# Kernel tuning notes

Hardware: AMD Instinct MI355X
Metric: run time of the kernel (lower is better)

## Reference

```python
import jax, jax.numpy as jnp
import numpy as np

EPS = 1e-6
D = 100   # embed_dim
P = 10    # perspective


def _cos(v1, v2):
    # cosine over last dim with broadcasting; clamp sum-of-squares at EPS (as torch)
    num = (v1 * v2).sum(-1)
    n1 = jnp.sqrt(jnp.clip((v1 * v1).sum(-1), EPS, None))
    n2 = jnp.sqrt(jnp.clip((v2 * v2).sum(-1), EPS, None))
    return num / (n1 * n2)


def _cosine_matrix(s1, s2):
    # [n1,B,D] x [n2,B,D] -> [n1,n2,B]; einsum avoids the [n1,n2,B,D] intermediate
    num = jnp.einsum('ibd,jbd->ijb', s1, s2)
    n1 = jnp.sqrt(jnp.clip((s1 * s1).sum(-1), EPS, None))  # [n1,B]
    n2 = jnp.sqrt(jnp.clip((s2 * s2).sum(-1), EPS, None))  # [n2,B]
    return num / (n1[:, None] * n2[None])


def _full(s1, s2, w):
    ws1 = s1[:, :, None, :] * w            # [n1,B,P,D]
    ws2 = s2[-1][:, None, :] * w           # [B,P,D]
    return _cos(ws1, ws2[None])            # [n1,B,P]


def _maxpool(s1, s2, w):
    # cos[i,j,b,p] between s1[i,b]*w[p] and s2[j,b]*w[p], without the 5-D intermediate
    w2 = w * w
    num = jnp.einsum('ibd,jbd,pd->ijbp', s1, s2, w2)
    n1 = jnp.sqrt(jnp.clip(jnp.einsum('ibd,pd->ibp', s1 * s1, w2), EPS, None))
    n2 = jnp.sqrt(jnp.clip(jnp.einsum('jbd,pd->jbp', s2 * s2, w2), EPS, None))
    cos = num / (n1[:, None] * n2[None])
    return cos.max(1)                      # [n1,B,P]


def _mean_att(s1, s2, w, cosm):
    # attentive vector: cosine-weighted mean of s2 states -> [n1,B,D]
    att = jnp.einsum('ijb,jbd->ibd', cosm, s2) / (cosm.sum(1) + EPS)[..., None]
    return _cos(s1[:, :, None, :] * w, att[:, :, None, :] * w)


def _max_att(s1, s2, w, cosm):
    n1, B = cosm.shape[0], s2.shape[1]
    idx = jnp.argmax(cosm, axis=1).reshape(-1)  # values in [0, n_state2)
    # NOTE: faithful to the torch source, which indexes the flattened [n2*B, D]
    # view of s2 with per-state indices (a bug in the original, reproduced here).
    att = s2.reshape(-1, D)[idx].reshape(n1, B, D)
    return _cos(s1[:, :, None, :] * w, att[:, :, None, :] * w)


def setup_inputs() -> dict:
    key = jax.random.key(0)
    ks = jax.random.split(key, 10)
    s1 = jax.random.normal(ks[0], (100, 256, 2 * D), dtype=jnp.float32)
    s2 = jax.random.normal(ks[1], (100, 256, 2 * D), dtype=jnp.float32)
    ws = {f'w{i+1}': jax.random.uniform(ks[2 + i], (P, D), dtype=jnp.float32,
                                        minval=-0.01, maxval=0.01) for i in range(8)}
    return {'s1': s1, 's2': s2, **ws}


def reference(s1, s2, w1, w2, w3, w4, w5, w6, w7, w8):
    s1f, s1b = s1[..., :D], s1[..., D:]
    s2f, s2b = s2[..., :D], s2[..., D:]
    cosf = _cosine_matrix(s1f, s2f)
    cosb = _cosine_matrix(s1b, s2b)
    full = jnp.concatenate([_full(s1f, s2f, w1), _full(s1b, s2b, w2)], 2)
    maxp = jnp.concatenate([_maxpool(s1f, s2f, w3), _maxpool(s1b, s2b, w4)], 2)
    mean_a = jnp.concatenate([_mean_att(s1f, s2f, w5, cosf), _mean_att(s1b, s2b, w6, cosb)], 2)
    # original forward uses mean_attentive for the backward half of max-attentive (bug kept)
    max_a = jnp.concatenate([_max_att(s1f, s2f, w7, cosf), _mean_att(s1b, s2b, w8, cosb)], 2)
    # `type` in the original forward shadows the builtin, so the 'all' branch always runs
    return jnp.concatenate([full, maxp, mean_a, max_a], axis=-1)  # [n1,B,8P]
```

## Files before the change

### kernel.cpp

```cpp
#include <hip/hip_runtime.h>

#define TT 100
#define DD 100
#define DC 25
#define PP 10
#define BBATCH 256
#define OC 80

typedef float v2f __attribute__((ext_vector_type(2)));
typedef float v4f __attribute__((ext_vector_type(4)));

static constexpr float FEPS = 1e-6f;

__device__ __forceinline__ float wsum(float v) {
#pragma unroll
  for (int m = 1; m < 64; m <<= 1) v += __shfl_xor(v, m, 64);
  return v;
}

__device__ __forceinline__ float wmaxr(float v) {
#pragma unroll
  for (int m = 1; m < 64; m <<= 1) v = fmaxf(v, __shfl_xor(v, m, 64));
  return v;
}

__device__ __forceinline__ void wargmax(float& v, int& idx) {
#pragma unroll
  for (int m = 1; m < 64; m <<= 1) {
    float ov = __shfl_xor(v, m, 64);
    int   oi = __shfl_xor(idx, m, 64);
    if (ov > v || (ov == v && oi < idx)) { v = ov; idx = oi; }
  }
}

__global__ __launch_bounds__(256, 2) void match_kernel(
    const float* __restrict__ s1, const float* __restrict__ s2,
    const float* __restrict__ w1, const float* __restrict__ w2,
    const float* __restrict__ w3, const float* __restrict__ w4,
    const float* __restrict__ w5, const float* __restrict__ w6,
    const float* __restrict__ w7, const float* __restrict__ w8,
    float* __restrict__ out)
{
  const int dir  = blockIdx.x & 1;
  const int b    = blockIdx.x >> 1;
  const int doff = dir * DD;
  const int tid  = threadIdx.x;
  const int lane = tid & 63;
  const int wv   = tid >> 6;

  const float* wfull = dir ? w2 : w1;
  const float* wmax  = dir ? w4 : w3;
  const float* wmean = dir ? w6 : w5;
  const float* watt2 = dir ? w8 : w7;

  __shared__ __align__(16) float S2V[DC][TT + 1][4];
  __shared__ __align__(16) float W2SQ[PP][DD];
  __shared__ float N2PI[TT];
  __shared__ float N2WI[TT][11];
  __shared__ __align__(16) float S1R[16][DD];
  __shared__ __align__(16) float CROW[16][DD];
  __shared__ float N1PI[16];
  __shared__ float N1WI[16][PP];
  __shared__ int   ARGJ[16];

  for (int idx = tid; idx < TT * DD; idx += 256) {
    int j = idx / DD, d = idx - j * DD;
    S2V[d >> 2][j][d & 3] = s2[(j * BBATCH + b) * (2 * DD) + doff + d];
  }
  for (int idx = tid; idx < PP * DD; idx += 256) {
    int p = idx / DD, d = idx - p * DD;
    float v = wmax[idx];
    W2SQ[p][d] = v * v;
  }
  __syncthreads();

  for (int task = tid; task < TT + TT * PP; task += 256) {
    if (task < TT) {
      int j = task;
      float a = 0.f;
      for (int c = 0; c < DC; ++c) {
        v4f f = *(const v4f*)&S2V[c][j][0];
#pragma unroll
        for (int k = 0; k < 4; ++k) a = fmaf(f[k], f[k], a);
      }
      N2PI[j] = 1.0f / sqrtf(fmaxf(a, FEPS));
    } else {
      int q = task - TT; int j = q / PP, p = q - j * PP;
      float a = 0.f;
      for (int c = 0; c < DC; ++c) {
        v4f f = *(const v4f*)&S2V[c][j][0];
        v4f w = *(const v4f*)&W2SQ[p][4 * c];
#pragma unroll
        for (int k = 0; k < 4; ++k) a = fmaf(f[k] * f[k], w[k], a);
      }
      N2WI[j][p] = rsqrtf(fmaxf(a, FEPS));
    }
  }
  __syncthreads();

  const int  j0   = lane;
  const int  j1   = 64 + lane;
  const bool act1 = (j1 < TT);
  const int  j1c  = act1 ? j1 : (TT - 1);
  const bool actd = (64 + lane) < DD;
  const int  d1   = actd ? (64 + lane) : (DD - 1);
  const int  c0i  = lane >> 2, k0 = lane & 3;
  const int  c1i  = d1 >> 2,   k1 = d1 & 3;

  for (int t = 0; t < 7; ++t) {
    const int rbase = t * 16;
    for (int idx = tid; idx < 16 * DD; idx += 256) {
      int r = idx / DD, d = idx - r * DD;
      int row = rbase + r;
      S1R[r][d] = (row < TT) ? s1[(row * BBATCH + b) * (2 * DD) + doff + d] : 0.f;
    }
    __syncthreads();

    for (int task = tid; task < 16 * 11; task += 256) {
      int rr = task / 11, q = task - rr * 11;
      if (q == 0) {
        float a = 0.f;
        for (int c = 0; c < DC; ++c) {
          v4f f = *(const v4f*)&S1R[rr][4 * c];
#pragma unroll
          for (int k = 0; k < 4; ++k) a = fmaf(f[k], f[k], a);
        }
        N1PI[rr] = 1.0f / sqrtf(fmaxf(a, FEPS));
      } else {
        int p = q - 1;
        float a = 0.f;
        for (int c = 0; c < DC; ++c) {
          v4f f = *(const v4f*)&S1R[rr][4 * c];
          v4f w = *(const v4f*)&W2SQ[p][4 * c];
#pragma unroll
          for (int k = 0; k < 4; ++k) a = fmaf(f[k] * f[k], w[k], a);
        }
        N1WI[rr][p] = rsqrtf(fmaxf(a, FEPS));
      }
    }
    __syncthreads();

    const int g = t * 4 + wv;
    const int i0 = g * 4;
    const int sl = wv * 4;
    const bool active = (g < 25);

    float rs[4] = {0, 0, 0, 0};
    v2f attp[4] = {{0, 0}, {0, 0}, {0, 0}, {0, 0}};

    if (active) {
      v2f dotp[4] = {{0, 0}, {0, 0}, {0, 0}, {0, 0}};
      v2f wap[4][PP];
#pragma unroll
      for (int r = 0; r < 4; ++r)
#pragma unroll
        for (int p = 0; p < PP; ++p) wap[r][p] = (v2f){0.f, 0.f};

      for (int c = 0; c < DC; ++c) {
        v4f s2a4 = *(const v4f*)&S2V[c][j0][0];
        v4f s2b4 = *(const v4f*)&S2V[c][j1c][0];
        v4f wq[PP];
#pragma unroll
        for (int p = 0; p < PP; ++p) wq[p] = *(const v4f*)&W2SQ[p][4 * c];
        v4f s1v[4];
#pragma unroll
        for (int r = 0; r < 4; ++r) s1v[r] = *(const v4f*)&S1R[sl + r][4 * c];
#pragma unroll
        for (int k = 0; k < 4; ++k) {
          v2f s2ab; s2ab.x = s2a4[k]; s2ab.y = s2b4[k];
#pragma unroll
          for (int r = 0; r < 4; ++r) {
            v2f s1xx; s1xx.x = s1v[r][k]; s1xx.y = s1v[r][k];
            v2f ta = s1xx * s2ab;
            dotp[r] += ta;
#pragma unroll
            for (int p = 0; p < PP; ++p) {
              v2f wk; wk.x = wq[p][k]; wk.y = wq[p][k];
              wap[r][p] = __builtin_elementwise_fma(ta, wk, wap[r][p]);
            }
          }
        }
      }

#pragma unroll
      for (int r = 0; r < 4; ++r) {
        float n1pi_r = N1PI[sl + r];
        float c0 = dotp[r].x * (n1pi_r * N2PI[j0]);
        float c1 = dotp[r].y * (n1pi_r * N2PI[j1c]);
        CROW[sl + r][j0] = c0;
        if (act1) CROW[sl + r][j1] = c1;
        rs[r] = wsum(c0 + (act1 ? c1 : 0.f));

        float mv = c0; int mi = j0;
        if (act1 && (c1 > mv)) { mv = c1; mi = j1; }
        wargmax(mv, mi);
        if (lane == 0) ARGJ[sl + r] = mi;

#pragma unroll
        for (int p = 0; p < PP; ++p) {
          float v0 = wap[r][p].x * N2WI[j0][p];
          float v1 = act1 ? wap[r][p].y * N2WI[j1c][p] : -3.4e38f;
          float m = wmaxr(fmaxf(v0, v1));
          if (lane == 0) {
            out[((i0 + r) * BBATCH + b) * OC + 20 + dir * PP + p] = m * N1WI[sl + r][p];
          }
        }
      }
    }
    __syncthreads();

    if (active) {
      for (int j = 0; j < TT; ++j) {
        v2f s2ab; s2ab.x = S2V[c0i][j][k0]; s2ab.y = S2V[c1i][j][k1];
#pragma unroll
        for (int r = 0; r < 4; ++r) {
          float cv = CROW[sl + r][j];
          v2f cc; cc.x = cv; cc.y = cv;
          attp[r] = __builtin_elementwise_fma(cc, s2ab, attp[r]);
        }
      }
    }
    __syncthreads();

    if (active) {
#pragma unroll
      for (int r = 0; r < 4; ++r) {
        float inv = 1.0f / (rs[r] + FEPS);
        CROW[sl + r][lane] = attp[r].x * inv;
        if (actd) CROW[sl + r][64 + lane] = attp[r].y * inv;
      }
    }
    __syncthreads();

    if (active) {
      for (int tk = lane; tk < 120; tk += 64) {
        int r = tk / 30;
        int q = tk - r * 30;
        int set = q / PP;
        int p = q - set * PP;
        const float* wrow = (set == 0 ? wfull : (set == 1 ? wmean : watt2)) + p * DD;
        const float* gat = s2 + ARGJ[sl + r] * (2 * DD);
        float num = 0.f, nx = 0.f, ny = 0.f;
        for (int c = 0; c < DC; ++c) {
          v4f x4 = *(const v4f*)&S1R[sl + r][4 * c];
          v4f y4;
          if (set == 0)                     y4 = *(const v4f*)&S2V[c][TT - 1][0];
          else if (set == 1 || dir == 1)    y4 = *(const v4f*)&CROW[sl + r][4 * c];
          else                              y4 = *(const v4f*)&gat[4 * c];
          v4f w4 = *(const v4f*)&wrow[4 * c];
#pragma unroll
          for (int k = 0; k < 4; ++k) {
            float w2v = w4[k] * w4[k];
            num = fmaf(x4[k] * y4[k], w2v, num);
            nx  = fmaf(x4[k] * x4[k], w2v, nx);
            ny  = fmaf(y4[k] * y4[k], w2v, ny);
          }
        }
        float cres = num * rsqrtf(fmaxf(nx, FEPS)) * rsqrtf(fmaxf(ny, FEPS));
        int ch = (set == 0 ? 0 : (set == 1 ? 40 : 60)) + dir * PP + p;
        out[((i0 + r) * BBATCH + b) * OC + ch] = cres;
      }
    }
    __syncthreads();
  }
}

extern "C" void kernel_launch(void* const* d_in, const int* in_sizes, int n_in,
                              void* d_out, int out_size, void* d_ws, size_t ws_size,
                              hipStream_t stream) {
  const float* s1 = (const float*)d_in[0];
  const float* s2 = (const float*)d_in[1];
  match_kernel<<<dim3(512), dim3(256), 0, stream>>>(
      s1, s2,
      (const float*)d_in[2], (const float*)d_in[3],
      (const float*)d_in[4], (const float*)d_in[5],
      (const float*)d_in[6], (const float*)d_in[7],
      (const float*)d_in[8], (const float*)d_in[9],
      (float*)d_out);
}
```

Baseline: 473.4 us.

## Split maxpool matching into separate bf16 MFMA kernel

Moves the maxpool perspective cosine out of the main fused kernel into its own kernel. The new kernel computes the weighted dot products per perspective as bf16 16x16x32 MFMA tiles, with s1 staged once and s2 scaled by w^2 and restaged per perspective. This removes the 40-accumulator FMA inner loop and its register pressure from the main kernel, which now only does plain cosine, attention and gather work with scalar FMAs. In exchange it adds a second launch, rereads s1/s2 from global memory, and uses bf16 inputs, so the max-pooled cosines lose precision.

Result: slower. 952.8 us (+101.3%).

```diff
diff --git a/kernel.cpp b/kernel.cpp
--- a/kernel.cpp
+++ b/kernel.cpp
@@ -6,21 +6,18 @@
 #define PP 10
 #define BBATCH 256
 #define OC 80
-
-typedef float v2f __attribute__((ext_vector_type(2)));
+#define KP 136
+
 typedef float v4f __attribute__((ext_vector_type(4)));
+typedef float v4fa __attribute__((ext_vector_type(4)));
+typedef short v8s __attribute__((ext_vector_type(8)));
 
 static constexpr float FEPS = 1e-6f;
+static constexpr float NEG_INF = -3.4e38f;
 
 __device__ __forceinline__ float wsum(float v) {
 #pragma unroll
   for (int m = 1; m < 64; m <<= 1) v += __shfl_xor(v, m, 64);
-  return v;
-}
-
-__device__ __forceinline__ float wmaxr(float v) {
-#pragma unroll
-  for (int m = 1; m < 64; m <<= 1) v = fmaxf(v, __shfl_xor(v, m, 64));
   return v;
 }
 
@@ -33,10 +30,15 @@
   }
 }
 
-__global__ __launch_bounds__(256, 2) void match_kernel(
+__device__ __forceinline__ unsigned short f2bf(float x) {
+  union { float f; unsigned u; } v; v.f = x;
+  unsigned r = v.u + 0x7FFF + ((v.u >> 16) & 1);
+  return (unsigned short)(r >> 16);
+}
+
+__global__ __launch_bounds__(256, 2) void match_main(
     const float* __restrict__ s1, const float* __restrict__ s2,
     const float* __restrict__ w1, const float* __restrict__ w2,
-    const float* __restrict__ w3, const float* __restrict__ w4,
     const float* __restrict__ w5, const float* __restrict__ w6,
     const float* __restrict__ w7, const float* __restrict__ w8,
     float* __restrict__ out)
@@ -49,52 +51,30 @@
   const int wv   = tid >> 6;
 
   const float* wfull = dir ? w2 : w1;
-  const float* wmax  = dir ? w4 : w3;
   const float* wmean = dir ? w6 : w5;
   const float* watt2 = dir ? w8 : w7;
 
   __shared__ __align__(16) float S2V[DC][TT + 1][4];
-  __shared__ __align__(16) float W2SQ[PP][DD];
-  __shared__ float N2PI[TT];
-  __shared__ float N2WI[TT][11];
   __shared__ __align__(16) float S1R[16][DD];
   __shared__ __align__(16) float CROW[16][DD];
+  __shared__ float N2PI[TT];
   __shared__ float N1PI[16];
-  __shared__ float N1WI[16][PP];
   __shared__ int   ARGJ[16];
 
   for (int idx = tid; idx < TT * DD; idx += 256) {
     int j = idx / DD, d = idx - j * DD;
     S2V[d >> 2][j][d & 3] = s2[(j * BBATCH + b) * (2 * DD) + doff + d];
   }
-  for (int idx = tid; idx < PP * DD; idx += 256) {
-    int p = idx / DD, d = idx - p * DD;
-    float v = wmax[idx];
-    W2SQ[p][d] = v * v;
-  }
   __syncthreads();
 
-  for (int task = tid; task < TT + TT * PP; task += 256) {
-    if (task < TT) {
-      int j = task;
-      float a = 0.f;
-      for (int c = 0; c < DC; ++c) {
-        v4f f = *(const v4f*)&S2V[c][j][0];
-#pragma unroll
-        for (int k = 0; k < 4; ++k) a = fmaf(f[k], f[k], a);
-      }
-      N2PI[j] = 1.0f / sqrtf(fmaxf(a, FEPS));
-    } else {
-      int q = task - TT; int j = q / PP, p = q - j * PP;
-      float a = 0.f;
-      for (int c = 0; c < DC; ++c) {
-        v4f f = *(const v4f*)&S2V[c][j][0];
-        v4f w = *(const v4f*)&W2SQ[p][4 * c];
-#pragma unroll
-        for (int k = 0; k < 4; ++k) a = fmaf(f[k] * f[k], w[k], a);
-      }
-      N2WI[j][p] = rsqrtf(fmaxf(a, FEPS));
-    }
+  for (int task = tid; task < TT; task += 256) {
+    float a = 0.f;
+    for (int c = 0; c < DC; ++c) {
+      v4f f = *(const v4f*)&S2V[c][task][0];
+#pragma unroll
+      for (int k = 0; k < 4; ++k) a = fmaf(f[k], f[k], a);
+    }
+    N2PI[task] = 1.0f / sqrtf(fmaxf(a, FEPS));
   }
   __syncthreads();
 
@@ -116,27 +96,14 @@
     }
     __syncthreads();
 
-    for (int task = tid; task < 16 * 11; task += 256) {
-      int rr = task / 11, q = task - rr * 11;
-      if (q == 0) {
-        float a = 0.f;
-        for (int c = 0; c < DC; ++c) {
-          v4f f = *(const v4f*)&S1R[rr][4 * c];
-#pragma unroll
-          for (int k = 0; k < 4; ++k) a = fmaf(f[k], f[k], a);
-        }
-        N1PI[rr] = 1.0f / sqrtf(fmaxf(a, FEPS));
-      } else {
-        int p = q - 1;
-        float a = 0.f;
-        for (int c = 0; c < DC; ++c) {
-          v4f f = *(const v4f*)&S1R[rr][4 * c];
-          v4f w = *(const v4f*)&W2SQ[p][4 * c];
-#pragma unroll
-          for (int k = 0; k < 4; ++k) a = fmaf(f[k] * f[k], w[k], a);
-        }
-        N1WI[rr][p] = rsqrtf(fmaxf(a, FEPS));
-      }
+    for (int task = tid; task < 16; task += 256) {
+      float a = 0.f;
+      for (int c = 0; c < DC; ++c) {
+        v4f f = *(const v4f*)&S1R[task][4 * c];
+#pragma unroll
+        for (int k = 0; k < 4; ++k) a = fmaf(f[k], f[k], a);
+      }
+      N1PI[task] = 1.0f / sqrtf(fmaxf(a, FEPS));
     }
     __syncthreads();
 
@@ -146,38 +113,22 @@
     const bool active = (g < 25);
 
     float rs[4] = {0, 0, 0, 0};
-    v2f attp[4] = {{0, 0}, {0, 0}, {0, 0}, {0, 0}};
+    float att0[4] = {0, 0, 0, 0}, att1[4] = {0, 0, 0, 0};
 
     if (active) {
-      v2f dotp[4] = {{0, 0}, {0, 0}, {0, 0}, {0, 0}};
-      v2f wap[4][PP];
-#pragma unroll
-      for (int r = 0; r < 4; ++r)
-#pragma unroll
-        for (int p = 0; p < PP; ++p) wap[r][p] = (v2f){0.f, 0.f};
-
+      float dot0[4] = {0, 0, 0, 0}, dot1[4] = {0, 0, 0, 0};
       for (int c = 0; c < DC; ++c) {
         v4f s2a4 = *(const v4f*)&S2V[c][j0][0];
         v4f s2b4 = *(const v4f*)&S2V[c][j1c][0];
-        v4f wq[PP];
-#pragma unroll
-        for (int p = 0; p < PP; ++p) wq[p] = *(const v4f*)&W2SQ[p][4 * c];
         v4f s1v[4];
 #pragma unroll
         for (int r = 0; r < 4; ++r) s1v[r] = *(const v4f*)&S1R[sl + r][4 * c];
 #pragma unroll
         for (int k = 0; k < 4; ++k) {
-          v2f s2ab; s2ab.x = s2a4[k]; s2ab.y = s2b4[k];
 #pragma unroll
           for (int r = 0; r < 4; ++r) {
-            v2f s1xx; s1xx.x = s1v[r][k]; s1xx.y = s1v[r][k];
-            v2f ta = s1xx * s2ab;
-            dotp[r] += ta;
-#pragma unroll
-            for (int p = 0; p < PP; ++p) {
-              v2f wk; wk.x = wq[p][k]; wk.y = wq[p][k];
-              wap[r][p] = __builtin_elementwise_fma(ta, wk, wap[r][p]);
-            }
+            dot0[r] = fmaf(s1v[r][k], s2a4[k], dot0[r]);
+            dot1[r] = fmaf(s1v[r][k], s2b4[k], dot1[r]);
           }
         }
       }
@@ -185,8 +136,8 @@
 #pragma unroll
       for (int r = 0; r < 4; ++r) {
         float n1pi_r = N1PI[sl + r];
-        float c0 = dotp[r].x * (n1pi_r * N2PI[j0]);
-        float c1 = dotp[r].y * (n1pi_r * N2PI[j1c]);
+        float c0 = dot0[r] * (n1pi_r * N2PI[j0]);
+        float c1 = dot1[r] * (n1pi_r * N2PI[j1c]);
         CROW[sl + r][j0] = c0;
         if (act1) CROW[sl + r][j1] = c1;
         rs[r] = wsum(c0 + (act1 ? c1 : 0.f));
@@ -195,28 +146,25 @@
         if (act1 && (c1 > mv)) { mv = c1; mi = j1; }
         wargmax(mv, mi);
         if (lane == 0) ARGJ[sl + r] = mi;
-
-#pragma unroll
-        for (int p = 0; p < PP; ++p) {
-          float v0 = wap[r][p].x * N2WI[j0][p];
-          float v1 = act1 ? wap[r][p].y * N2WI[j1c][p] : -3.4e38f;
-          float m = wmaxr(fmaxf(v0, v1));
-          if (lane == 0) {
-            out[((i0 + r) * BBATCH + b) * OC + 20 + dir * PP + p] = m * N1WI[sl + r][p];
+      }
+    }
+    __syncthreads();
+
+    if (active) {
+      for (int jb = 0; jb < TT; jb += 4) {
+        v4f cr[4];
+#pragma unroll
+        for (int r = 0; r < 4; ++r) cr[r] = *(const v4f*)&CROW[sl + r][jb];
+#pragma unroll
+        for (int q = 0; q < 4; ++q) {
+          int j = jb + q;
+          float s2a = S2V[c0i][j][k0];
+          float s2b = S2V[c1i][j][k1];
+#pragma unroll
+          for (int r = 0; r < 4; ++r) {
+            att0[r] = fmaf(cr[r][q], s2a, att0[r]);
+            att1[r] = fmaf(cr[r][q], s2b, att1[r]);
           }
-        }
-      }
-    }
-    __syncthreads();
-
-    if (active) {
-      for (int j = 0; j < TT; ++j) {
-        v2f s2ab; s2ab.x = S2V[c0i][j][k0]; s2ab.y = S2V[c1i][j][k1];
-#pragma unroll
-        for (int r = 0; r < 4; ++r) {
-          float cv = CROW[sl + r][j];
-          v2f cc; cc.x = cv; cc.y = cv;
-          attp[r] = __builtin_elementwise_fma(cc, s2ab, attp[r]);
         }
       }
     }
@@ -226,8 +174,8 @@
 #pragma unroll
       for (int r = 0; r < 4; ++r) {
         float inv = 1.0f / (rs[r] + FEPS);
-        CROW[sl + r][lane] = attp[r].x * inv;
-        if (actd) CROW[sl + r][64 + lane] = attp[r].y * inv;
+        CROW[sl + r][lane] = att0[r] * inv;
+        if (actd) CROW[sl + r][64 + lane] = att1[r] * inv;
       }
     }
     __syncthreads();
@@ -244,9 +192,9 @@
         for (int c = 0; c < DC; ++c) {
           v4f x4 = *(const v4f*)&S1R[sl + r][4 * c];
           v4f y4;
-          if (set == 0)                     y4 = *(const v4f*)&S2V[c][TT - 1][0];
-          else if (set == 1 || dir == 1)    y4 = *(const v4f*)&CROW[sl + r][4 * c];
-          else                              y4 = *(const v4f*)&gat[4 * c];
+          if (set == 0)                  y4 = *(const v4f*)&S2V[c][TT - 1][0];
+          else if (set == 1 || dir == 1) y4 = *(const v4f*)&CROW[sl + r][4 * c];
+          else                           y4 = *(const v4f*)&gat[4 * c];
           v4f w4 = *(const v4f*)&wrow[4 * c];
 #pragma unroll
           for (int k = 0; k < 4; ++k) {
@@ -265,16 +213,125 @@
   }
 }
 
+__global__ __launch_bounds__(256, 2) void maxpool_mfma(
+    const float* __restrict__ s1, const float* __restrict__ s2,
+    const float* __restrict__ w3, const float* __restrict__ w4,
+    float* __restrict__ out)
+{
+  const int dir  = blockIdx.x & 1;
+  const int b    = blockIdx.x >> 1;
+  const int doff = dir * DD;
+  const float* wmax = dir ? w4 : w3;
+  const int tid  = threadIdx.x;
+  const int lane = tid & 63;
+  const int wv   = tid >> 6;
+  const int quad = lane >> 4;
+  const int col  = lane & 15;
+
+  __shared__ __align__(16) unsigned short Abf[TT][KP];
+  __shared__ __align__(16) unsigned short Bbf[TT][KP];
+  __shared__ float N1W[TT][PP];
+  __shared__ float N2Wp[112];
+
+  for (int idx = tid; idx < TT * KP; idx += 256) {
+    int i = idx / KP, q = idx - i * KP;
+    float v = (q < DD) ? s1[(i * BBATCH + b) * (2 * DD) + doff + q] : 0.f;
+    Abf[i][q] = f2bf(v);
+  }
+  for (int task = tid; task < TT * PP; task += 256) {
+    int i = task / PP, p = task - i * PP;
+    const float* s1r = s1 + (i * BBATCH + b) * (2 * DD) + doff;
+    const float* wr  = wmax + p * DD;
+    float a = 0.f;
+    for (int c = 0; c < DC; ++c) {
+      v4f x = *(const v4f*)&s1r[4 * c];
+      v4f w = *(const v4f*)&wr[4 * c];
+#pragma unroll
+      for (int k = 0; k < 4; ++k) a = fmaf(x[k] * x[k], w[k] * w[k], a);
+    }
+    N1W[i][p] = rsqrtf(fmaxf(a, FEPS));
+  }
+  __syncthreads();
+
+  for (int p = 0; p < PP; ++p) {
+    const float* wr = wmax + p * DD;
+    for (int idx = tid; idx < TT * KP; idx += 256) {
+      int j = idx / KP, q = idx - j * KP;
+      float v = 0.f;
+      if (q < DD) { float w = wr[q]; v = s2[(j * BBATCH + b) * (2 * DD) + doff + q] * (w * w); }
+      Bbf[j][q] = f2bf(v);
+    }
+    for (int task = tid; task < 112; task += 256) {
+      float a = 0.f;
+      if (task < TT) {
+        const float* s2r = s2 + (task * BBATCH + b) * (2 * DD) + doff;
+        for (int c = 0; c < DC; ++c) {
+          v4f x = *(const v4f*)&s2r[4 * c];
+          v4f w = *(const v4f*)&wr[4 * c];
+#pragma unroll
+          for (int k = 0; k < 4; ++k) a = fmaf(x[k] * x[k], w[k] * w[k], a);
+        }
+        N2Wp[task] = rsqrtf(fmaxf(a, FEPS));
+      } else {
+        N2Wp[task] = 0.f;
+      }
+    }
+    __syncthreads();
+
+    for (int it = wv; it < 7; it += 4) {
+      int arow = min(it * 16 + col, TT - 1);
+      v8s afr[4];
+#pragma unroll
+      for (int kc = 0; kc < 4; ++kc)
+        afr[kc] = *(const v8s*)&Abf[arow][kc * 32 + quad * 8];
+
+      float rmax[4] = {NEG_INF, NEG_INF, NEG_INF, NEG_INF};
+      for (int jt = 0; jt < 7; ++jt) {
+        int brow = min(jt * 16 + col, TT - 1);
+        v4fa acc = {0.f, 0.f, 0.f, 0.f};
+#pragma unroll
+        for (int kc = 0; kc < 4; ++kc) {
+          v8s bfr = *(const v8s*)&Bbf[brow][kc * 32 + quad * 8];
+          acc = __builtin_amdgcn_mfma_f32_16x16x32_bf16(afr[kc], bfr, acc, 0, 0, 0);
+        }
+        int jcol = jt * 16 + col;
+        if (jcol < TT) {
+          float n2 = N2Wp[jcol];
+#pragma unroll
+          for (int r = 0; r < 4; ++r) rmax[r] = fmaxf(rmax[r], acc[r] * n2);
+        }
+      }
+#pragma unroll
+      for (int m = 1; m < 16; m <<= 1) {
+#pragma unroll
+        for (int r = 0; r < 4; ++r) rmax[r] = fmaxf(rmax[r], __shfl_xor(rmax[r], m, 64));
+      }
+      if (col == 0) {
+#pragma unroll
+        for (int r = 0; r < 4; ++r) {
+          int row = it * 16 + quad * 4 + r;
+          if (row < TT)
+            out[(row * BBATCH + b) * OC + 20 + dir * PP + p] = rmax[r] * N1W[row][p];
+        }
+      }
+    }
+    __syncthreads();
+  }
+}
+
 extern "C" void kernel_launch(void* const* d_in, const int* in_sizes, int n_in,
                               void* d_out, int out_size, void* d_ws, size_t ws_size,
                               hipStream_t stream) {
   const float* s1 = (const float*)d_in[0];
   const float* s2 = (const float*)d_in[1];
-  match_kernel<<<dim3(512), dim3(256), 0, stream>>>(
+  match_main<<<dim3(512), dim3(256), 0, stream>>>(
       s1, s2,
       (const float*)d_in[2], (const float*)d_in[3],
-      (const float*)d_in[4], (const float*)d_in[5],
       (const float*)d_in[6], (const float*)d_in[7],
       (const float*)d_in[8], (const float*)d_in[9],
       (float*)d_out);
-}
+  maxpool_mfma<<<dim3(512), dim3(256), 0, stream>>>(
+      s1, s2,
+      (const float*)d_in[4], (const float*)d_in[5],
+      (float*)d_out);
+}
```

## Compute maxpool weighted cosine numerators with bf16 MFMA instead of scalar FMA

Applied to the files above, without the earlier changes.

Removes the per-lane weighted accumulation (40 FMAs per element per row) for the maxpool perspective matching. Instead it builds bf16 A fragments from s1*w^2 and B fragments from s2 and runs 16x16x32 bf16 MFMA tiles over j, then takes a running max and a 16-lane shuffle reduction. This moves the dominant FLOPs onto matrix cores and lowers register pressure. In exchange it adds bf16 rounding error on the maxpool outputs.

Result: slower. 791.0 us (+67.1%).

```diff
diff --git a/kernel.cpp b/kernel.cpp
--- a/kernel.cpp
+++ b/kernel.cpp
@@ -9,18 +9,15 @@
 
 typedef float v2f __attribute__((ext_vector_type(2)));
 typedef float v4f __attribute__((ext_vector_type(4)));
+typedef short v8s __attribute__((ext_vector_type(8)));
+typedef unsigned v4u __attribute__((ext_vector_type(4)));
 
 static constexpr float FEPS = 1e-6f;
+static constexpr float NEG_INF = -3.4e38f;
 
 __device__ __forceinline__ float wsum(float v) {
 #pragma unroll
   for (int m = 1; m < 64; m <<= 1) v += __shfl_xor(v, m, 64);
-  return v;
-}
-
-__device__ __forceinline__ float wmaxr(float v) {
-#pragma unroll
-  for (int m = 1; m < 64; m <<= 1) v = fmaxf(v, __shfl_xor(v, m, 64));
   return v;
 }
 
@@ -31,6 +28,14 @@
     int   oi = __shfl_xor(idx, m, 64);
     if (ov > v || (ov == v && oi < idx)) { v = ov; idx = oi; }
   }
+}
+
+__device__ __forceinline__ unsigned pkbf(float lo, float hi) {
+  unsigned a = __float_as_uint(lo);
+  unsigned b = __float_as_uint(hi);
+  a += 0x7FFFu + ((a >> 16) & 1u);
+  b += 0x7FFFu + ((b >> 16) & 1u);
+  return (a >> 16) | (b & 0xFFFF0000u);
 }
 
 __global__ __launch_bounds__(256, 2) void match_kernel(
@@ -68,9 +73,8 @@
     S2V[d >> 2][j][d & 3] = s2[(j * BBATCH + b) * (2 * DD) + doff + d];
   }
   for (int idx = tid; idx < PP * DD; idx += 256) {
-    int p = idx / DD, d = idx - p * DD;
     float v = wmax[idx];
-    W2SQ[p][d] = v * v;
+    W2SQ[idx / DD][idx - (idx / DD) * DD] = v * v;
   }
   __syncthreads();
 
@@ -150,18 +154,10 @@
 
     if (active) {
       v2f dotp[4] = {{0, 0}, {0, 0}, {0, 0}, {0, 0}};
-      v2f wap[4][PP];
-#pragma unroll
-      for (int r = 0; r < 4; ++r)
-#pragma unroll
-        for (int p = 0; p < PP; ++p) wap[r][p] = (v2f){0.f, 0.f};
 
       for (int c = 0; c < DC; ++c) {
         v4f s2a4 = *(const v4f*)&S2V[c][j0][0];
         v4f s2b4 = *(const v4f*)&S2V[c][j1c][0];
-        v4f wq[PP];
-#pragma unroll
-        for (int p = 0; p < PP; ++p) wq[p] = *(const v4f*)&W2SQ[p][4 * c];
         v4f s1v[4];
 #pragma unroll
         for (int r = 0; r < 4; ++r) s1v[r] = *(const v4f*)&S1R[sl + r][4 * c];
@@ -171,13 +167,7 @@
 #pragma unroll
           for (int r = 0; r < 4; ++r) {
             v2f s1xx; s1xx.x = s1v[r][k]; s1xx.y = s1v[r][k];
-            v2f ta = s1xx * s2ab;
-            dotp[r] += ta;
-#pragma unroll
-            for (int p = 0; p < PP; ++p) {
-              v2f wk; wk.x = wq[p][k]; wk.y = wq[p][k];
-              wap[r][p] = __builtin_elementwise_fma(ta, wk, wap[r][p]);
-            }
+            dotp[r] += s1xx * s2ab;
           }
         }
       }
@@ -195,14 +185,96 @@
         if (act1 && (c1 > mv)) { mv = c1; mi = j1; }
         wargmax(mv, mi);
         if (lane == 0) ARGJ[sl + r] = mi;
-
-#pragma unroll
-        for (int p = 0; p < PP; ++p) {
-          float v0 = wap[r][p].x * N2WI[j0][p];
-          float v1 = act1 ? wap[r][p].y * N2WI[j1c][p] : -3.4e38f;
-          float m = wmaxr(fmaxf(v0, v1));
-          if (lane == 0) {
-            out[((i0 + r) * BBATCH + b) * OC + 20 + dir * PP + p] = m * N1WI[sl + r][p];
+      }
+    }
+
+    {
+      const int col = lane & 15;
+      const int qd  = lane >> 4;
+      const v4f vz = {0.f, 0.f, 0.f, 0.f};
+
+      v4u afr[3][4];
+      float rmax[3][4];
+#pragma unroll
+      for (int pi = 0; pi < 3; ++pi) {
+        const int p = (wv + 4 * pi < PP) ? (wv + 4 * pi) : (PP - 1);
+#pragma unroll
+        for (int kc = 0; kc < 4; ++kc) {
+          v4f x0, x1, w0, w1;
+          if (kc < 3) {
+            int d0 = kc * 32 + qd * 8;
+            x0 = *(const v4f*)&S1R[col][d0];
+            x1 = *(const v4f*)&S1R[col][d0 + 4];
+            w0 = *(const v4f*)&W2SQ[p][d0];
+            w1 = *(const v4f*)&W2SQ[p][d0 + 4];
+          } else {
+            bool ok = (qd == 0);
+            x0 = ok ? *(const v4f*)&S1R[col][96] : vz;
+            w0 = ok ? *(const v4f*)&W2SQ[p][96] : vz;
+            x1 = vz; w1 = vz;
+          }
+          v4u f;
+          f.x = pkbf(x0[0] * w0[0], x0[1] * w0[1]);
+          f.y = pkbf(x0[2] * w0[2], x0[3] * w0[3]);
+          f.z = pkbf(x1[0] * w1[0], x1[1] * w1[1]);
+          f.w = pkbf(x1[2] * w1[2], x1[3] * w1[3]);
+          afr[pi][kc] = f;
+        }
+#pragma unroll
+        for (int r = 0; r < 4; ++r) rmax[pi][r] = NEG_INF;
+      }
+
+      for (int jt = 0; jt < 7; ++jt) {
+        int jr = jt * 16 + col;
+        int jc = (jr < TT) ? jr : (TT - 1);
+        v4u bfr[4];
+#pragma unroll
+        for (int kc = 0; kc < 4; ++kc) {
+          int ch = kc * 8 + qd * 2;
+          int ch0 = (ch     <= 24) ? ch     : 24;
+          int ch1 = (ch + 1 <= 24) ? ch + 1 : 24;
+          v4f y0 = (ch     <= 24) ? *(const v4f*)&S2V[ch0][jc][0] : vz;
+          v4f y1 = (ch + 1 <= 24) ? *(const v4f*)&S2V[ch1][jc][0] : vz;
+          v4u f;
+          f.x = pkbf(y0[0], y0[1]); f.y = pkbf(y0[2], y0[3]);
+          f.z = pkbf(y1[0], y1[1]); f.w = pkbf(y1[2], y1[3]);
+          bfr[kc] = f;
+        }
+#pragma unroll
+        for (int pi = 0; pi < 3; ++pi) {
+          const int p = (wv + 4 * pi < PP) ? (wv + 4 * pi) : (PP - 1);
+          v4f acc = {0.f, 0.f, 0.f, 0.f};
+#pragma unroll
+          for (int kc = 0; kc < 4; ++kc)
+            acc = __builtin_amdgcn_mfma_f32_16x16x32_bf16(
+                __builtin_bit_cast(v8s, afr[pi][kc]),
+                __builtin_bit_cast(v8s, bfr[kc]), acc, 0, 0, 0);
+          if (jr < TT) {
+            float n2 = N2WI[jr][p];
+#pragma unroll
+            for (int r = 0; r < 4; ++r)
+              rmax[pi][r] = fmaxf(rmax[pi][r], acc[r] * n2);
+          }
+        }
+      }
+#pragma unroll
+      for (int pi = 0; pi < 3; ++pi) {
+        const int p = wv + 4 * pi;
+        if (p < PP) {
+#pragma unroll
+          for (int m = 1; m < 16; m <<= 1)
+#pragma unroll
+            for (int r = 0; r < 4; ++r)
+              rmax[pi][r] = fmaxf(rmax[pi][r], __shfl_xor(rmax[pi][r], m, 64));
+          if (col == 0) {
+#pragma unroll
+            for (int r = 0; r < 4; ++r) {
+              int lrow = qd * 4 + r;
+              int row = rbase + lrow;
+              if (row < TT)
+                out[(row * BBATCH + b) * OC + 20 + dir * PP + p] =
+                    rmax[pi][r] * N1WI[lrow][p];
+            }
           }
         }
       }
```
